# Kernel optimization log

Hardware: AMD Instinct MI355X
Metric: run time of the kernel (lower is better)

## Reference

```python
import jax, jax.numpy as jnp
import numpy as np

T, H, I, E, SI, TOP_K = 1024, 2048, 1408, 60, 5632, 4


def setup_inputs() -> dict:
    key = jax.random.key(0)
    ks = jax.random.split(key, 9)
    s = 0.02  # typical init scale for weights
    return {
        "x": jax.random.normal(ks[0], (T, H), jnp.float32),
        "router_w": jax.random.normal(ks[1], (E, H), jnp.float32) * s,
        "w_gate": jax.random.normal(ks[2], (E, I, H), jnp.float32) * s,
        "w_up": jax.random.normal(ks[3], (E, I, H), jnp.float32) * s,
        "w_down": jax.random.normal(ks[4], (E, H, I), jnp.float32) * s,
        "sw_gate": jax.random.normal(ks[5], (SI, H), jnp.float32) * s,
        "sw_up": jax.random.normal(ks[6], (SI, H), jnp.float32) * s,
        "sw_down": jax.random.normal(ks[7], (H, SI), jnp.float32) * s,
        "shared_gate_w": jax.random.normal(ks[8], (1, H), jnp.float32) * s,
        "top_k": TOP_K,
    }


def reference(x, router_w, w_gate, w_up, w_down, sw_gate, sw_up, sw_down, shared_gate_w, top_k):
    Ttok, Hdim = x.shape
    Eexp = router_w.shape[0]
    # --- router: softmax over experts, top-k selection (norm_topk_prob=False) ---
    logits = x @ router_w.T                          # [T,E]
    probs = jax.nn.softmax(logits, axis=-1)
    topk_p, topk_i = jax.lax.top_k(probs, top_k)     # [T,k]
    # dense combine weights: zero for unrouted experts
    combine = jnp.zeros((Ttok, Eexp), x.dtype)
    combine = combine.at[jnp.arange(Ttok)[:, None], topk_i].set(topk_p)  # [T,E]

    # --- routed experts: SwiGLU MLP per expert, weighted accumulate (scan over E) ---
    def expert_step(acc, w):
        wg, wu, wd, c = w                            # [I,H],[I,H],[H,I],[T]
        h = jax.nn.silu(x @ wg.T) * (x @ wu.T)       # [T,I]
        return acc + c[:, None] * (h @ wd.T), None

    moe_out, _ = jax.lax.scan(expert_step, jnp.zeros_like(x),
                              (w_gate, w_up, w_down, combine.T))

    # --- shared expert with sigmoid gate ---
    shared = (jax.nn.silu(x @ sw_gate.T) * (x @ sw_up.T)) @ sw_down.T    # [T,H]
    shared = jax.nn.sigmoid(x @ shared_gate_w.T) * shared                # [T,1]*[T,H]
    return moe_out + shared
```

## Files before the change

### kernel.cpp

```cpp
#include <hip/hip_runtime.h>
#include <hip/hip_bf16.h>


typedef float  f32x4  __attribute__((ext_vector_type(4)));
typedef short  bf16x8 __attribute__((ext_vector_type(8)));
typedef unsigned short u16;
typedef unsigned int   u32;

constexpr int TT = 1024, HD = 2048, ID = 1408, NE = 60, SID = 5632, KTOP = 4;
constexpr int NBR_GU = (ID / 64) * NE;
constexpr int NB_GU  = NBR_GU + (SID / 64) * (TT / 128);
constexpr int NBS_DN = (HD / 64) * (TT / 128);
constexpr int NB_DN  = NBS_DN + (HD / 64) * NE;

#define GLDS(g, l) __builtin_amdgcn_global_load_lds( \
    (const __attribute__((address_space(1))) void*)(g), \
    (__attribute__((address_space(3))) void*)(l), 16, 0, 0)
#define WAITVM(n) asm volatile("s_waitcnt vmcnt(" #n ")" ::: "memory")
#define BAR() do { asm volatile("" ::: "memory"); \
    __builtin_amdgcn_s_barrier(); \
    asm volatile("" ::: "memory"); } while (0)

__device__ __forceinline__ u16 f2bf(float f) {
    union { float f; u32 u; } v; v.f = f;
    u32 r = v.u + 0x7FFFu + ((v.u >> 16) & 1u);
    return (u16)(r >> 16);
}
__device__ __forceinline__ u32 cvtpk(float a, float b) {
    u32 r; asm("v_cvt_pk_bf16_f32 %0, %1, %2" : "=v"(r) : "v"(a), "v"(b));
    return r;
}
__device__ __forceinline__ bf16x8 cvt8(float4 a, float4 b) {
    union { u32 u[4]; bf16x8 v; } rr;
    rr.u[0] = cvtpk(a.x, a.y); rr.u[1] = cvtpk(a.z, a.w);
    rr.u[2] = cvtpk(b.x, b.y); rr.u[3] = cvtpk(b.z, b.w);
    return rr.v;
}

__global__ void zero_k(int* __restrict__ p) { p[threadIdx.x] = 0; }

__global__ __launch_bounds__(256) void zeroout_k(float* __restrict__ p) {
    ((float4*)p)[blockIdx.x * 256 + threadIdx.x] = make_float4(0.f, 0.f, 0.f, 0.f);
}

__global__ __launch_bounds__(256) void xcvt_k(const float* __restrict__ x, u16* __restrict__ xb)
{
    size_t i = ((size_t)blockIdx.x * 256 + threadIdx.x) * 16;
    const float4* p = (const float4*)(x + i);
    float4 f0 = p[0], f1 = p[1], f2 = p[2], f3 = p[3];
    uint4 o0, o1;
    o0.x = cvtpk(f0.x, f0.y); o0.y = cvtpk(f0.z, f0.w);
    o0.z = cvtpk(f1.x, f1.y); o0.w = cvtpk(f1.z, f1.w);
    o1.x = cvtpk(f2.x, f2.y); o1.y = cvtpk(f2.z, f2.w);
    o1.z = cvtpk(f3.x, f3.y); o1.w = cvtpk(f3.z, f3.w);
    ((uint4*)(xb + i))[0] = o0;
    ((uint4*)(xb + i))[1] = o1;
}

__global__ __launch_bounds__(64) void router_k(
    const float* __restrict__ x, const float* __restrict__ rw,
    const float* __restrict__ sgw,
    float* __restrict__ topk_p, int* __restrict__ topk_i,
    int* __restrict__ cnt, float* __restrict__ sgate)
{
    const int t = blockIdx.x, l = threadIdx.x;
    const float4* xr = ((const float4*)(x + (size_t)t * HD)) + l * 8;
    float4 xa[8];
    #pragma unroll
    for (int i = 0; i < 8; i++) xa[i] = xr[i];

    float le = 0.f;
    for (int e = 0; e < NE; e++) {
        const float4* wr = ((const float4*)(rw + (size_t)e * HD)) + l * 8;
        float a = 0.f;
        #pragma unroll
        for (int i = 0; i < 8; i++) {
            float4 wv = wr[i];
            a += xa[i].x * wv.x + xa[i].y * wv.y + xa[i].z * wv.z + xa[i].w * wv.w;
        }
        #pragma unroll
        for (int s = 32; s; s >>= 1) a += __shfl_xor(a, s);
        if (l == e) le = a;
    }
    {
        const float4* wr = ((const float4*)sgw) + l * 8;
        float a = 0.f;
        #pragma unroll
        for (int i = 0; i < 8; i++) {
            float4 wv = wr[i];
            a += xa[i].x * wv.x + xa[i].y * wv.y + xa[i].z * wv.z + xa[i].w * wv.w;
        }
        #pragma unroll
        for (int s = 32; s; s >>= 1) a += __shfl_xor(a, s);
        if (l == 0) sgate[t] = 1.f / (1.f + __expf(-a));
    }
    float mv = (l < NE) ? le : -3.4e38f;
    #pragma unroll
    for (int s = 32; s; s >>= 1) mv = fmaxf(mv, __shfl_xor(mv, s));
    float p = (l < NE) ? __expf(le - mv) : 0.f;
    float ss = p;
    #pragma unroll
    for (int s = 32; s; s >>= 1) ss += __shfl_xor(ss, s);
    p /= ss;
    float pv = (l < NE) ? p : -1.f;
    int   pi = l;
    float kp = 0.f; int ki = 0;
    for (int k = 0; k < KTOP; k++) {
        float bv = pv; int bi = pi;
        #pragma unroll
        for (int s = 32; s; s >>= 1) {
            float ov = __shfl_xor(bv, s); int oi = __shfl_xor(bi, s);
            if (ov > bv || (ov == bv && oi < bi)) { bv = ov; bi = oi; }
        }
        if (l == k) { kp = bv; ki = bi; }
        if (pi == bi) pv = -1.f;
    }
    if (l < KTOP) {
        topk_p[t * KTOP + l] = kp;
        topk_i[t * KTOP + l] = ki;
        atomicAdd(&cnt[ki], 1);
    }
}

__global__ __launch_bounds__(64) void prefix_k(const int* __restrict__ cnt, int* __restrict__ base)
{
    int l = threadIdx.x;
    if (l < NE) {
        int s = 0;
        for (int j = 0; j < l; j++) s += cnt[j];
        base[l] = s;
    }
}

__global__ __launch_bounds__(256) void scatter_k(
    const float* __restrict__ topk_p, const int* __restrict__ topk_i,
    const int* __restrict__ base, int* __restrict__ fill,
    int* __restrict__ slot_tok, float* __restrict__ slot_wt)
{
    int t = blockIdx.x * blockDim.x + threadIdx.x;
    if (t >= TT) return;
    for (int k = 0; k < KTOP; k++) {
        int e = topk_i[t * KTOP + k];
        int pos = atomicAdd(&fill[e], 1);
        int s = base[e] + pos;
        slot_tok[s] = t;
        slot_wt[s]  = topk_p[t * KTOP + k];
    }
}

__global__ __launch_bounds__(256, 3) void gu_all(
    const u16* __restrict__ Xb,
    const float* __restrict__ w_gate, const float* __restrict__ w_up,
    const float* __restrict__ sw_g, const float* __restrict__ sw_u,
    u16* __restrict__ h, u16* __restrict__ hs,
    const int* __restrict__ slot_tok, const float* __restrict__ slot_wt,
    const int* __restrict__ cnt, const int* __restrict__ basea)
{
    __shared__ u16   Asl[2][128 * 32];
    __shared__ float Bgsl[2][64 * 32];
    __shared__ float Busl[2][64 * 32];

    const int bid = blockIdx.x;
    const bool grouped = bid < NBR_GU;
    const int tid = threadIdx.x, w = tid >> 6, lane = tid & 63;
    const int lm = lane & 15, lk = lane >> 4;
    const int wm0 = (w >> 1) * 64, wn0 = (w & 1) * 32;

    int e = 0, my = 0, nb;
    const float *Wg, *Wu; u16* Hout; int Nout;
    if (grouped) {
        e = bid / 22; nb = bid % 22;
        Wg = w_gate + (size_t)e * ID * HD; Wu = w_up + (size_t)e * ID * HD;
        Hout = h; Nout = ID;
    } else {
        int sid = bid - NBR_GU; my = sid / 88; nb = sid % 88;
        Wg = sw_g; Wu = sw_u; Hout = hs; Nout = SID;
    }
    const int mcnt  = grouped ? cnt[e] : 128;
    const int mbase = grouped ? basea[e] : 0;

    const int aCh = (((lane & 3) ^ ((lane >> 2) & 3) ^ ((lane >> 4) & 3))) << 3;
    const int bCh = ((lane & 7) ^ ((lane >> 3) & 7)) << 2;

    const float* bgSrc[2]; const float* buSrc[2];
    #pragma unroll
    for (int j = 0; j < 2; j++) {
        size_t rB = (size_t)(nb * 64 + w * 16 + j * 8 + (lane >> 3));
        bgSrc[j] = Wg + rB * HD + bCh;
        buSrc[j] = Wu + rB * HD + bCh;
    }

    int aOff[4], bOff[2][2];
    #pragma unroll
    for (int mf = 0; mf < 4; mf++) {
        int r = wm0 + mf * 16 + lm;
        aOff[mf] = r * 32 + ((lk ^ (r & 3) ^ ((r >> 2) & 3)) << 3);
    }
    #pragma unroll
    for (int nf = 0; nf < 2; nf++) {
        int rb = wn0 + nf * 16 + lm;
        bOff[nf][0] = rb * 32 + ((((lk << 1)    ) ^ (rb & 7)) << 2);
        bOff[nf][1] = rb * 32 + ((((lk << 1) | 1) ^ (rb & 7)) << 2);
    }

    const int nk = HD >> 5;

    for (int mt = 0; grouped ? (mt * 128 < mcnt) : (mt == 0); ++mt) {
        const u16* aSrc[2];
        #pragma unroll
        for (int j = 0; j < 2; j++) {
            int mrow = w * 32 + j * 16 + (lane >> 2);
            int row;
            if (grouped) {
                int sl = mbase + mt * 128 + mrow;
                row = (mt * 128 + mrow < mcnt) ? slot_tok[sl] : slot_tok[mbase];
            } else row = my * 128 + mrow;
            aSrc[j] = Xb + (size_t)row * HD + aCh;
        }

        f32x4 accG[4][2], accU[4][2];
        #pragma unroll
        for (int mf = 0; mf < 4; mf++)
            #pragma unroll
            for (int nf = 0; nf < 2; nf++) {
                accG[mf][nf] = f32x4{0.f, 0.f, 0.f, 0.f};
                accU[mf][nf] = f32x4{0.f, 0.f, 0.f, 0.f};
            }

        auto stage = [&](int b, int kt) {
            #pragma unroll
            for (int j = 0; j < 2; j++)
                GLDS(aSrc[j] + kt, &Asl[b][(w * 32 + j * 16) * 32]);
            #pragma unroll
            for (int j = 0; j < 2; j++) {
                GLDS(bgSrc[j] + kt, &Bgsl[b][(w * 16 + j * 8) * 32]);
                GLDS(buSrc[j] + kt, &Busl[b][(w * 16 + j * 8) * 32]);
            }
        };

        stage(0, 0);
        for (int t = 0; t < nk; ++t) {
            const int cur = t & 1;
            if (t + 1 < nk) { stage(cur ^ 1, (t + 1) << 5); WAITVM(6); }
            else WAITVM(0);
            BAR();
            const u16*   At  = Asl[cur];
            const float* Bgt = Bgsl[cur];
            const float* But = Busl[cur];
            bf16x8 af[4];
            #pragma unroll
            for (int mf = 0; mf < 4; mf++) af[mf] = *(const bf16x8*)&At[aOff[mf]];
            #pragma unroll
            for (int nf = 0; nf < 2; nf++) {
                bf16x8 bg = cvt8(*(const float4*)&Bgt[bOff[nf][0]],
                                 *(const float4*)&Bgt[bOff[nf][1]]);
                bf16x8 bu = cvt8(*(const float4*)&But[bOff[nf][0]],
                                 *(const float4*)&But[bOff[nf][1]]);
                #pragma unroll
                for (int mf = 0; mf < 4; mf++) {
                    accG[mf][nf] = __builtin_amdgcn_mfma_f32_16x16x32_bf16(af[mf], bg, accG[mf][nf], 0, 0, 0);
                    accU[mf][nf] = __builtin_amdgcn_mfma_f32_16x16x32_bf16(af[mf], bu, accU[mf][nf], 0, 0, 0);
                }
            }
            BAR();
        }

        #pragma unroll
        for (int mf = 0; mf < 4; mf++)
            #pragma unroll
            for (int j = 0; j < 4; j++) {
                int m = wm0 + mf * 16 + lk * 4 + j;
                bool valid = grouped ? (mt * 128 + m < mcnt) : true;
                if (valid) {
                    size_t row; float wt;
                    if (grouped) {
                        size_t sl = (size_t)(mbase + mt * 128 + m);
                        row = sl; wt = slot_wt[sl];
                    } else { row = (size_t)(my * 128 + m); wt = 1.f; }
                    #pragma unroll
                    for (int nf = 0; nf < 2; nf++) {
                        int col = nb * 64 + wn0 + nf * 16 + lm;
                        float g = accG[mf][nf][j], u = accU[mf][nf][j];
                        float hv = g / (1.f + __expf(-g)) * u * wt;
                        Hout[row * (size_t)Nout + col] = f2bf(hv);
                    }
                }
            }
    }
}

__global__ __launch_bounds__(256, 3) void down_all(
    const u16* __restrict__ h, const u16* __restrict__ hs,
    const float* __restrict__ w_down, const float* __restrict__ sw_d,
    float* __restrict__ outF,
    const int* __restrict__ slot_tok, const float* __restrict__ sgate,
    const int* __restrict__ cnt, const int* __restrict__ basea)
{
    __shared__ u16   Asl[3][128 * 32];
    __shared__ float Bsl[3][64 * 32];

    const int bid = blockIdx.x;
    const bool shared_m = bid < NBS_DN;
    const int tid = threadIdx.x, w = tid >> 6, lane = tid & 63;
    const int lm = lane & 15, lk = lane >> 4;
    const int wm0 = (w >> 1) * 64, wn0 = (w & 1) * 32;

    int e = 0, my = 0, nb, K;
    const u16* Ap; const float* Wp;
    if (shared_m) {
        my = bid / 32; nb = bid % 32; K = SID; Ap = hs; Wp = sw_d;
    } else {
        int rid = bid - NBS_DN; e = rid / 32; nb = rid % 32; K = ID;
        Ap = h; Wp = w_down + (size_t)e * HD * ID;
    }
    const int mcnt  = shared_m ? 128 : cnt[e];
    const int mbase = shared_m ? 0 : basea[e];

    const int aCh = (((lane & 3) ^ ((lane >> 2) & 3) ^ ((lane >> 4) & 3))) << 3;
    const int bCh = ((lane & 7) ^ ((lane >> 3) & 7)) << 2;

    const float* bSrc[2];
    #pragma unroll
    for (int j = 0; j < 2; j++) {
        size_t rB = (size_t)(nb * 64 + w * 16 + j * 8 + (lane >> 3));
        bSrc[j] = Wp + rB * K + bCh;
    }

    int aOff[4], bOff[2][2];
    #pragma unroll
    for (int mf = 0; mf < 4; mf++) {
        int r = wm0 + mf * 16 + lm;
        aOff[mf] = r * 32 + ((lk ^ (r & 3) ^ ((r >> 2) & 3)) << 3);
    }
    #pragma unroll
    for (int nf = 0; nf < 2; nf++) {
        int rb = wn0 + nf * 16 + lm;
        bOff[nf][0] = rb * 32 + ((((lk << 1)    ) ^ (rb & 7)) << 2);
        bOff[nf][1] = rb * 32 + ((((lk << 1) | 1) ^ (rb & 7)) << 2);
    }

    const int nk = K >> 5;

    for (int mt = 0; shared_m ? (mt == 0) : (mt * 128 < mcnt); ++mt) {
        const u16* aSrc[2];
        #pragma unroll
        for (int j = 0; j < 2; j++) {
            int mrow = w * 32 + j * 16 + (lane >> 2);
            size_t row = shared_m ? (size_t)(my * 128 + mrow)
                                  : (size_t)(mbase + mt * 128 + mrow);
            aSrc[j] = Ap + row * K + aCh;
        }

        f32x4 acc[4][2];
        #pragma unroll
        for (int mf = 0; mf < 4; mf++)
            #pragma unroll
            for (int nf = 0; nf < 2; nf++) acc[mf][nf] = f32x4{0.f, 0.f, 0.f, 0.f};

        auto stage = [&](int b, int kt) {
            #pragma unroll
            for (int j = 0; j < 2; j++)
                GLDS(aSrc[j] + kt, &Asl[b][(w * 32 + j * 16) * 32]);
            #pragma unroll
            for (int j = 0; j < 2; j++)
                GLDS(bSrc[j] + kt, &Bsl[b][(w * 16 + j * 8) * 32]);
        };
        auto comp = [&](int b) {
            const u16*   At = Asl[b];
            const float* Bt = Bsl[b];
            bf16x8 af[4];
            #pragma unroll
            for (int mf = 0; mf < 4; mf++) af[mf] = *(const bf16x8*)&At[aOff[mf]];
            #pragma unroll
            for (int nf = 0; nf < 2; nf++) {
                bf16x8 bf_ = cvt8(*(const float4*)&Bt[bOff[nf][0]],
                                  *(const float4*)&Bt[bOff[nf][1]]);
                #pragma unroll
                for (int mf = 0; mf < 4; mf++)
                    acc[mf][nf] = __builtin_amdgcn_mfma_f32_16x16x32_bf16(af[mf], bf_, acc[mf][nf], 0, 0, 0);
            }
        };

        stage(0, 0); stage(1, 32);
        int t = 0, cb = 0;
        for (; t + 2 < nk; ++t) {
            int sbuf = cb - 1; if (sbuf < 0) sbuf += 3;
            stage(sbuf, (t + 2) << 5);
            WAITVM(8); BAR(); comp(cb); BAR();
            cb = (cb + 1 == 3) ? 0 : cb + 1;
        }
        WAITVM(4); BAR(); comp(cb); BAR();
        cb = (cb + 1 == 3) ? 0 : cb + 1;
        WAITVM(0); BAR(); comp(cb); BAR();

        #pragma unroll
        for (int mf = 0; mf < 4; mf++)
            #pragma unroll
            for (int j = 0; j < 4; j++) {
                int m = wm0 + mf * 16 + lk * 4 + j;
                if (mt * 128 + m < mcnt) {
                    int tok; float scale;
                    if (shared_m) { tok = my * 128 + m; scale = sgate[tok]; }
                    else          { tok = slot_tok[mbase + mt * 128 + m]; scale = 1.f; }
                    #pragma unroll
                    for (int nf = 0; nf < 2; nf++) {
                        int col = nb * 64 + wn0 + nf * 16 + lm;
                        atomicAdd(&outF[(size_t)tok * HD + col], scale * acc[mf][nf][j]);
                    }
                }
            }
    }
}

extern "C" void kernel_launch(void* const* d_in, const int* in_sizes, int n_in,
                              void* d_out, int out_size, void* d_ws, size_t ws_size,
                              hipStream_t stream)
{
    const float* x      = (const float*)d_in[0];
    const float* rw     = (const float*)d_in[1];
    const float* w_gate = (const float*)d_in[2];
    const float* w_up   = (const float*)d_in[3];
    const float* w_down = (const float*)d_in[4];
    const float* sw_g   = (const float*)d_in[5];
    const float* sw_u   = (const float*)d_in[6];
    const float* sw_d   = (const float*)d_in[7];
    const float* sgw    = (const float*)d_in[8];
    float* out = (float*)d_out;

    char* ws = (char*)d_ws;
    int*   cnt      = (int*)(ws + 0);
    int*   fill     = (int*)(ws + 256);
    int*   basea    = (int*)(ws + 512);
    float* sgate    = (float*)(ws + 768);
    float* topk_p   = (float*)(ws + 5120);
    int*   topk_i   = (int*)(ws + 21504);
    int*   slot_tok = (int*)(ws + 37888);
    float* slot_wt  = (float*)(ws + 54272);
    u16*   xb = (u16*)(ws + 71680);
    u16*   h  = xb + (size_t)TT * HD;
    u16*   hs = h + (size_t)(4096 + 128) * ID;

    zero_k<<<1, 128, 0, stream>>>(cnt);
    zeroout_k<<<TT * HD / 1024, 256, 0, stream>>>(out);
    xcvt_k<<<512, 256, 0, stream>>>(x, xb);
    router_k<<<TT, 64, 0, stream>>>(x, rw, sgw, topk_p, topk_i, cnt, sgate);
    prefix_k<<<1, 64, 0, stream>>>(cnt, basea);
    scatter_k<<<4, 256, 0, stream>>>(topk_p, topk_i, basea, fill, slot_tok, slot_wt);

    gu_all<<<NB_GU, 256, 0, stream>>>(
        xb, w_gate, w_up, sw_g, sw_u, h, hs,
        slot_tok, slot_wt, cnt, basea);

    down_all<<<NB_DN, 256, 0, stream>>>(
        h, hs, w_down, sw_d, out,
        slot_tok, sgate, cnt, basea);
}
```

Before: 727.8 us.

## Load GEMM operands directly into registers, dropping LDS staging and barriers

Both the gate/up and down GEMM kernels stop staging A and B tiles through shared memory with global_load_lds. Each wave now loads its own MFMA fragments straight into VGPRs with inline-asm dwordx4 loads, double-buffered in registers, with no block barriers. This removes LDS traffic and synchronisation, but blocks no longer share tiles, so waves in the same block fetch duplicate data from global memory or cache. The larger register footprint is handled by lowering the launch-bounds occupancy hint from 3 to 2.

Measured after the change: 1.321 ms. +81.4%, slower.

```diff
diff --git a/kernel.cpp b/kernel.cpp
--- a/kernel.cpp
+++ b/kernel.cpp
@@ -3,6 +3,7 @@
 
 
 typedef float  f32x4  __attribute__((ext_vector_type(4)));
+typedef unsigned int u32x4 __attribute__((ext_vector_type(4)));
 typedef short  bf16x8 __attribute__((ext_vector_type(8)));
 typedef unsigned short u16;
 typedef unsigned int   u32;
@@ -13,13 +14,9 @@
 constexpr int NBS_DN = (HD / 64) * (TT / 128);
 constexpr int NB_DN  = NBS_DN + (HD / 64) * NE;
 
-#define GLDS(g, l) __builtin_amdgcn_global_load_lds( \
-    (const __attribute__((address_space(1))) void*)(g), \
-    (__attribute__((address_space(3))) void*)(l), 16, 0, 0)
-#define WAITVM(n) asm volatile("s_waitcnt vmcnt(" #n ")" ::: "memory")
-#define BAR() do { asm volatile("" ::: "memory"); \
-    __builtin_amdgcn_s_barrier(); \
-    asm volatile("" ::: "memory"); } while (0)
+#define GL4(dst, ptr) asm volatile("global_load_dwordx4 %0, %1, off" : "=&v"(dst) : "v"(ptr))
+#define WAITVM(n) do { asm volatile("s_waitcnt vmcnt(" #n ")" ::: "memory"); \
+                       __builtin_amdgcn_sched_barrier(0); } while (0)
 
 __device__ __forceinline__ u16 f2bf(float f) {
     union { float f; u32 u; } v; v.f = f;
@@ -30,11 +27,14 @@
     u32 r; asm("v_cvt_pk_bf16_f32 %0, %1, %2" : "=v"(r) : "v"(a), "v"(b));
     return r;
 }
-__device__ __forceinline__ bf16x8 cvt8(float4 a, float4 b) {
+__device__ __forceinline__ bf16x8 cvt8(f32x4 a, f32x4 b) {
     union { u32 u[4]; bf16x8 v; } rr;
-    rr.u[0] = cvtpk(a.x, a.y); rr.u[1] = cvtpk(a.z, a.w);
-    rr.u[2] = cvtpk(b.x, b.y); rr.u[3] = cvtpk(b.z, b.w);
+    rr.u[0] = cvtpk(a[0], a[1]); rr.u[1] = cvtpk(a[2], a[3]);
+    rr.u[2] = cvtpk(b[0], b[1]); rr.u[3] = cvtpk(b[2], b[3]);
     return rr.v;
+}
+__device__ __forceinline__ bf16x8 asbf(u32x4 v) {
+    union { u32x4 u; bf16x8 b; } c; c.u = v; return c.b;
 }
 
 __global__ void zero_k(int* __restrict__ p) { p[threadIdx.x] = 0; }
@@ -148,7 +148,7 @@
     }
 }
 
-__global__ __launch_bounds__(256, 3) void gu_all(
+__global__ __launch_bounds__(256, 2) void gu_all(
     const u16* __restrict__ Xb,
     const float* __restrict__ w_gate, const float* __restrict__ w_up,
     const float* __restrict__ sw_g, const float* __restrict__ sw_u,
@@ -156,10 +156,6 @@
     const int* __restrict__ slot_tok, const float* __restrict__ slot_wt,
     const int* __restrict__ cnt, const int* __restrict__ basea)
 {
-    __shared__ u16   Asl[2][128 * 32];
-    __shared__ float Bgsl[2][64 * 32];
-    __shared__ float Busl[2][64 * 32];
-
     const int bid = blockIdx.x;
     const bool grouped = bid < NBR_GU;
     const int tid = threadIdx.x, w = tid >> 6, lane = tid & 63;
@@ -178,44 +174,27 @@
     }
     const int mcnt  = grouped ? cnt[e] : 128;
     const int mbase = grouped ? basea[e] : 0;
-
-    const int aCh = (((lane & 3) ^ ((lane >> 2) & 3) ^ ((lane >> 4) & 3))) << 3;
-    const int bCh = ((lane & 7) ^ ((lane >> 3) & 7)) << 2;
-
-    const float* bgSrc[2]; const float* buSrc[2];
-    #pragma unroll
-    for (int j = 0; j < 2; j++) {
-        size_t rB = (size_t)(nb * 64 + w * 16 + j * 8 + (lane >> 3));
-        bgSrc[j] = Wg + rB * HD + bCh;
-        buSrc[j] = Wu + rB * HD + bCh;
-    }
-
-    int aOff[4], bOff[2][2];
-    #pragma unroll
-    for (int mf = 0; mf < 4; mf++) {
-        int r = wm0 + mf * 16 + lm;
-        aOff[mf] = r * 32 + ((lk ^ (r & 3) ^ ((r >> 2) & 3)) << 3);
-    }
-    #pragma unroll
-    for (int nf = 0; nf < 2; nf++) {
-        int rb = wn0 + nf * 16 + lm;
-        bOff[nf][0] = rb * 32 + ((((lk << 1)    ) ^ (rb & 7)) << 2);
-        bOff[nf][1] = rb * 32 + ((((lk << 1) | 1) ^ (rb & 7)) << 2);
-    }
-
     const int nk = HD >> 5;
 
     for (int mt = 0; grouped ? (mt * 128 < mcnt) : (mt == 0); ++mt) {
-        const u16* aSrc[2];
-        #pragma unroll
-        for (int j = 0; j < 2; j++) {
-            int mrow = w * 32 + j * 16 + (lane >> 2);
+        const u16* pa0[4]; const u16* pa1[4];
+        #pragma unroll
+        for (int mf = 0; mf < 4; mf++) {
+            int mrow = wm0 + mf * 16 + lm;
             int row;
             if (grouped) {
                 int sl = mbase + mt * 128 + mrow;
                 row = (mt * 128 + mrow < mcnt) ? slot_tok[sl] : slot_tok[mbase];
             } else row = my * 128 + mrow;
-            aSrc[j] = Xb + (size_t)row * HD + aCh;
+            pa0[mf] = Xb + (size_t)row * HD + lk * 8;
+            pa1[mf] = pa0[mf] + 32;
+        }
+        const float *pg0[2], *pg1[2], *pu0[2], *pu1[2];
+        #pragma unroll
+        for (int nf = 0; nf < 2; nf++) {
+            size_t row = (size_t)(nb * 64 + wn0 + nf * 16 + lm);
+            pg0[nf] = Wg + row * HD + lk * 8; pg1[nf] = pg0[nf] + 32;
+            pu0[nf] = Wu + row * HD + lk * 8; pu1[nf] = pu0[nf] + 32;
         }
 
         f32x4 accG[4][2], accU[4][2];
@@ -227,43 +206,45 @@
                 accU[mf][nf] = f32x4{0.f, 0.f, 0.f, 0.f};
             }
 
-        auto stage = [&](int b, int kt) {
-            #pragma unroll
-            for (int j = 0; j < 2; j++)
-                GLDS(aSrc[j] + kt, &Asl[b][(w * 32 + j * 16) * 32]);
-            #pragma unroll
-            for (int j = 0; j < 2; j++) {
-                GLDS(bgSrc[j] + kt, &Bgsl[b][(w * 16 + j * 8) * 32]);
-                GLDS(buSrc[j] + kt, &Busl[b][(w * 16 + j * 8) * 32]);
-            }
-        };
-
-        stage(0, 0);
-        for (int t = 0; t < nk; ++t) {
-            const int cur = t & 1;
-            if (t + 1 < nk) { stage(cur ^ 1, (t + 1) << 5); WAITVM(6); }
-            else WAITVM(0);
-            BAR();
-            const u16*   At  = Asl[cur];
-            const float* Bgt = Bgsl[cur];
-            const float* But = Busl[cur];
-            bf16x8 af[4];
-            #pragma unroll
-            for (int mf = 0; mf < 4; mf++) af[mf] = *(const bf16x8*)&At[aOff[mf]];
-            #pragma unroll
-            for (int nf = 0; nf < 2; nf++) {
-                bf16x8 bg = cvt8(*(const float4*)&Bgt[bOff[nf][0]],
-                                 *(const float4*)&Bgt[bOff[nf][1]]);
-                bf16x8 bu = cvt8(*(const float4*)&But[bOff[nf][0]],
-                                 *(const float4*)&But[bOff[nf][1]]);
-                #pragma unroll
-                for (int mf = 0; mf < 4; mf++) {
-                    accG[mf][nf] = __builtin_amdgcn_mfma_f32_16x16x32_bf16(af[mf], bg, accG[mf][nf], 0, 0, 0);
-                    accU[mf][nf] = __builtin_amdgcn_mfma_f32_16x16x32_bf16(af[mf], bu, accU[mf][nf], 0, 0, 0);
-                }
-            }
-            BAR();
-        }
+        u32x4 A0[4], A1[4];
+        f32x4 G0[4], G1[4], U0[4], U1[4];
+
+#define LOADP(A_, G_, U_, PA_, PG_, PU_) do {                                  \
+        GL4(A_[0], PA_[0]); GL4(A_[1], PA_[1]);                                \
+        GL4(A_[2], PA_[2]); GL4(A_[3], PA_[3]);                                \
+        GL4(G_[0], PG_[0]); GL4(G_[1], PG_[0] + 4);                            \
+        GL4(G_[2], PG_[1]); GL4(G_[3], PG_[1] + 4);                            \
+        GL4(U_[0], PU_[0]); GL4(U_[1], PU_[0] + 4);                            \
+        GL4(U_[2], PU_[1]); GL4(U_[3], PU_[1] + 4);                            \
+        PA_[0] += 64; PA_[1] += 64; PA_[2] += 64; PA_[3] += 64;                \
+        PG_[0] += 64; PG_[1] += 64; PU_[0] += 64; PU_[1] += 64;                \
+    } while (0)
+
+#define COMPP(A_, G_, U_) do {                                                 \
+        bf16x8 bg0 = cvt8(G_[0], G_[1]), bg1 = cvt8(G_[2], G_[3]);             \
+        bf16x8 bu0 = cvt8(U_[0], U_[1]), bu1 = cvt8(U_[2], U_[3]);             \
+        _Pragma("unroll")                                                      \
+        for (int mf = 0; mf < 4; mf++) {                                       \
+            bf16x8 af = asbf(A_[mf]);                                          \
+            accG[mf][0] = __builtin_amdgcn_mfma_f32_16x16x32_bf16(af, bg0, accG[mf][0], 0, 0, 0); \
+            accG[mf][1] = __builtin_amdgcn_mfma_f32_16x16x32_bf16(af, bg1, accG[mf][1], 0, 0, 0); \
+            accU[mf][0] = __builtin_amdgcn_mfma_f32_16x16x32_bf16(af, bu0, accU[mf][0], 0, 0, 0); \
+            accU[mf][1] = __builtin_amdgcn_mfma_f32_16x16x32_bf16(af, bu1, accU[mf][1], 0, 0, 0); \
+        }                                                                      \
+    } while (0)
+
+        LOADP(A0, G0, U0, pa0, pg0, pu0);
+        for (int t = 0; t + 2 < nk; t += 2) {
+            LOADP(A1, G1, U1, pa1, pg1, pu1);
+            WAITVM(12); COMPP(A0, G0, U0);
+            LOADP(A0, G0, U0, pa0, pg0, pu0);
+            WAITVM(12); COMPP(A1, G1, U1);
+        }
+        LOADP(A1, G1, U1, pa1, pg1, pu1);
+        WAITVM(12); COMPP(A0, G0, U0);
+        WAITVM(0);  COMPP(A1, G1, U1);
+#undef LOADP
+#undef COMPP
 
         #pragma unroll
         for (int mf = 0; mf < 4; mf++)
@@ -289,16 +270,13 @@
     }
 }
 
-__global__ __launch_bounds__(256, 3) void down_all(
+__global__ __launch_bounds__(256, 2) void down_all(
     const u16* __restrict__ h, const u16* __restrict__ hs,
     const float* __restrict__ w_down, const float* __restrict__ sw_d,
     float* __restrict__ outF,
     const int* __restrict__ slot_tok, const float* __restrict__ sgate,
     const int* __restrict__ cnt, const int* __restrict__ basea)
 {
-    __shared__ u16   Asl[3][128 * 32];
-    __shared__ float Bsl[3][64 * 32];
-
     const int bid = blockIdx.x;
     const bool shared_m = bid < NBS_DN;
     const int tid = threadIdx.x, w = tid >> 6, lane = tid & 63;
@@ -315,40 +293,23 @@
     }
     const int mcnt  = shared_m ? 128 : cnt[e];
     const int mbase = shared_m ? 0 : basea[e];
-
-    const int aCh = (((lane & 3) ^ ((lane >> 2) & 3) ^ ((lane >> 4) & 3))) << 3;
-    const int bCh = ((lane & 7) ^ ((lane >> 3) & 7)) << 2;
-
-    const float* bSrc[2];
-    #pragma unroll
-    for (int j = 0; j < 2; j++) {
-        size_t rB = (size_t)(nb * 64 + w * 16 + j * 8 + (lane >> 3));
-        bSrc[j] = Wp + rB * K + bCh;
-    }
-
-    int aOff[4], bOff[2][2];
-    #pragma unroll
-    for (int mf = 0; mf < 4; mf++) {
-        int r = wm0 + mf * 16 + lm;
-        aOff[mf] = r * 32 + ((lk ^ (r & 3) ^ ((r >> 2) & 3)) << 3);
-    }
-    #pragma unroll
-    for (int nf = 0; nf < 2; nf++) {
-        int rb = wn0 + nf * 16 + lm;
-        bOff[nf][0] = rb * 32 + ((((lk << 1)    ) ^ (rb & 7)) << 2);
-        bOff[nf][1] = rb * 32 + ((((lk << 1) | 1) ^ (rb & 7)) << 2);
-    }
-
     const int nk = K >> 5;
 
     for (int mt = 0; shared_m ? (mt == 0) : (mt * 128 < mcnt); ++mt) {
-        const u16* aSrc[2];
-        #pragma unroll
-        for (int j = 0; j < 2; j++) {
-            int mrow = w * 32 + j * 16 + (lane >> 2);
+        const u16* pa0[4]; const u16* pa1[4];
+        #pragma unroll
+        for (int mf = 0; mf < 4; mf++) {
+            int mrow = wm0 + mf * 16 + lm;
             size_t row = shared_m ? (size_t)(my * 128 + mrow)
                                   : (size_t)(mbase + mt * 128 + mrow);
-            aSrc[j] = Ap + row * K + aCh;
+            pa0[mf] = Ap + row * K + lk * 8;
+            pa1[mf] = pa0[mf] + 32;
+        }
+        const float *pb0[2], *pb1[2];
+        #pragma unroll
+        for (int nf = 0; nf < 2; nf++) {
+            size_t row = (size_t)(nb * 64 + wn0 + nf * 16 + lm);
+            pb0[nf] = Wp + row * K + lk * 8; pb1[nf] = pb0[nf] + 32;
         }
 
         f32x4 acc[4][2];
@@ -357,41 +318,40 @@
             #pragma unroll
             for (int nf = 0; nf < 2; nf++) acc[mf][nf] = f32x4{0.f, 0.f, 0.f, 0.f};
 
-        auto stage = [&](int b, int kt) {
-            #pragma unroll
-            for (int j = 0; j < 2; j++)
-                GLDS(aSrc[j] + kt, &Asl[b][(w * 32 + j * 16) * 32]);
-            #pragma unroll
-            for (int j = 0; j < 2; j++)
-                GLDS(bSrc[j] + kt, &Bsl[b][(w * 16 + j * 8) * 32]);
-        };
-        auto comp = [&](int b) {
-            const u16*   At = Asl[b];
-            const float* Bt = Bsl[b];
-            bf16x8 af[4];
-            #pragma unroll
-            for (int mf = 0; mf < 4; mf++) af[mf] = *(const bf16x8*)&At[aOff[mf]];
-            #pragma unroll
-            for (int nf = 0; nf < 2; nf++) {
-                bf16x8 bf_ = cvt8(*(const float4*)&Bt[bOff[nf][0]],
-                                  *(const float4*)&Bt[bOff[nf][1]]);
-                #pragma unroll
-                for (int mf = 0; mf < 4; mf++)
-                    acc[mf][nf] = __builtin_amdgcn_mfma_f32_16x16x32_bf16(af[mf], bf_, acc[mf][nf], 0, 0, 0);
-            }
-        };
-
-        stage(0, 0); stage(1, 32);
-        int t = 0, cb = 0;
-        for (; t + 2 < nk; ++t) {
-            int sbuf = cb - 1; if (sbuf < 0) sbuf += 3;
-            stage(sbuf, (t + 2) << 5);
-            WAITVM(8); BAR(); comp(cb); BAR();
-            cb = (cb + 1 == 3) ? 0 : cb + 1;
-        }
-        WAITVM(4); BAR(); comp(cb); BAR();
-        cb = (cb + 1 == 3) ? 0 : cb + 1;
-        WAITVM(0); BAR(); comp(cb); BAR();
+        u32x4 A0[4], A1[4];
+        f32x4 B0[4], B1[4];
+
+#define LOADP(A_, B_, PA_, PB_) do {                                           \
+        GL4(A_[0], PA_[0]); GL4(A_[1], PA_[1]);                                \
+        GL4(A_[2], PA_[2]); GL4(A_[3], PA_[3]);                                \
+        GL4(B_[0], PB_[0]); GL4(B_[1], PB_[0] + 4);                            \
+        GL4(B_[2], PB_[1]); GL4(B_[3], PB_[1] + 4);                            \
+        PA_[0] += 64; PA_[1] += 64; PA_[2] += 64; PA_[3] += 64;                \
+        PB_[0] += 64; PB_[1] += 64;                                            \
+    } while (0)
+
+#define COMPP(A_, B_) do {                                                     \
+        bf16x8 b0 = cvt8(B_[0], B_[1]), b1 = cvt8(B_[2], B_[3]);               \
+        _Pragma("unroll")                                                      \
+        for (int mf = 0; mf < 4; mf++) {                                       \
+            bf16x8 af = asbf(A_[mf]);                                          \
+            acc[mf][0] = __builtin_amdgcn_mfma_f32_16x16x32_bf16(af, b0, acc[mf][0], 0, 0, 0); \
+            acc[mf][1] = __builtin_amdgcn_mfma_f32_16x16x32_bf16(af, b1, acc[mf][1], 0, 0, 0); \
+        }                                                                      \
+    } while (0)
+
+        LOADP(A0, B0, pa0, pb0);
+        for (int t = 0; t + 2 < nk; t += 2) {
+            LOADP(A1, B1, pa1, pb1);
+            WAITVM(8); COMPP(A0, B0);
+            LOADP(A0, B0, pa0, pb0);
+            WAITVM(8); COMPP(A1, B1);
+        }
+        LOADP(A1, B1, pa1, pb1);
+        WAITVM(8); COMPP(A0, B0);
+        WAITVM(0); COMPP(A1, B1);
+#undef LOADP
+#undef COMPP
 
         #pragma unroll
         for (int mf = 0; mf < 4; mf++)
```
